# Optimization experiments

Hardware: AMD Instinct MI355X
Metric: run time of the kernel (lower is better)

Reference implementation:

```python
import jax, jax.numpy as jnp
import numpy as np

B, C, H, W = 8, 256, 64, 64
CR = C // 8  # reduced channels = 32


def setup_inputs() -> dict:
    key = jax.random.key(0)
    k1, k2, k3, k4 = jax.random.split(key, 4)
    x = jax.random.normal(k1, (B, C, H, W), dtype=jnp.float32)
    # 1x1 conv weights (bias=False) are plain channel matmuls; scale like kaiming (~1/sqrt(fan_in))
    Wt = jax.random.normal(k2, (3 * CR, C), dtype=jnp.float32) * (1.0 / np.sqrt(C))
    Wo = jax.random.normal(k3, (C, CR), dtype=jnp.float32) * (1.0 / np.sqrt(CR))
    scale = jax.random.normal(k4, (1,), dtype=jnp.float32)
    return {"x": x, "Wt": Wt, "Wo": Wo, "scale": scale}


def reference(x, Wt, Wo, scale):
    b, c, h, w = x.shape
    n = h * w
    # 1x1 conv QKV projection: [B, 3*Cr, H, W]
    t = jnp.einsum('oc,bchw->bohw', Wt, x)
    cr = t.shape[1] // 3
    key = t[:, :cr].reshape(b, cr, n)          # [B, Cr, N]
    query = t[:, cr:2 * cr].reshape(b, cr, n)  # [B, Cr, N]
    value = t[:, 2 * cr:].reshape(b, cr, n)    # [B, Cr, N]
    # scores[b, i, j] = sum_c key[b,c,i] * query[b,c,j]  (key^T @ query)
    scores = jnp.einsum('bci,bcj->bij', key, query)  # [B, N, N]
    # torch Softmax(dim=1): normalize over the key axis i
    weights = jax.nn.softmax(scores, axis=1)
    # output[b, c, j] = sum_i value[b,c,i] * weights[b,i,j]
    out = jnp.einsum('bci,bij->bcj', value, weights)  # [B, Cr, N]
    out = out.reshape(b, cr, h, w)
    out = jnp.einsum('oc,bchw->bohw', Wo, out)  # 1x1 conv back to C channels
    return scale[0] * out + x
```

## Files before the change

kernel.cpp:

```cpp
#include <hip/hip_runtime.h>
#include <math.h>

#define B_ 8
#define C_ 256
#define CR_ 32
#define N_ 4096
#define KSPLIT 8

typedef __attribute__((ext_vector_type(8))) short bf16x8;
typedef __attribute__((ext_vector_type(4))) short bf16x4;
typedef __attribute__((ext_vector_type(4))) float f32x4;
typedef __attribute__((ext_vector_type(16))) float f32x16;

__device__ inline short f2bf(float f) {
  union { float f; unsigned u; } v; v.f = f;
  unsigned r = v.u + 0x7FFFu + ((v.u >> 16) & 1u);
  return (short)(r >> 16);
}
__device__ inline float bf2f(short h) {
  union { unsigned u; float f; } v; v.u = ((unsigned)(unsigned short)h) << 16;
  return v.f;
}
__device__ inline short f2bf_r(float f) {
  return (short)((__float_as_uint(f) + 0x8000u) >> 16);
}

__global__ __launch_bounds__(256) void prep_weights(const float* __restrict__ Wt,
                                                    const float* __restrict__ Wo,
                                                    const float* __restrict__ scale,
                                                    short* __restrict__ WtHi,
                                                    short* __restrict__ WtLo,
                                                    short* __restrict__ WoB) {
  const int blk = blockIdx.x, tid = threadIdx.x;
  if (blk < 96) {
    float v = Wt[blk * C_ + tid];
    if (blk >= 32 && blk < 64) v *= 1.44269504f;
    const short h = f2bf(v);
    WtHi[blk * C_ + tid] = h;
    WtLo[blk * C_ + tid] = f2bf(v - bf2f(h));
  } else {
    const int idx = (blk - 96) * 256 + tid;
    WoB[idx] = f2bf(Wo[idx] * scale[0]);
  }
}

__global__ __launch_bounds__(256) void qkv_mfma(const float* __restrict__ x,
                                                const short* __restrict__ WtHi,
                                                const short* __restrict__ WtLo,
                                                short* __restrict__ t_tr,
                                                short* __restrict__ Vg) {
  const int b = blockIdx.y;
  const int tid = threadIdx.x;
  const int wave = tid >> 6, lane = tid & 63;
  const int pair = wave >> 1, chalf = wave & 1;
  const int col = lane & 15, quad = lane >> 4;
  const int n0 = (blockIdx.x * 2 + pair) * 16;
  const int cbase = chalf * 128;

  __shared__ float Ms[2][64][25];

  const f32x4 z4 = {0.f, 0.f, 0.f, 0.f};
  f32x4 acc[6] = {z4, z4, z4, z4, z4, z4};

  const float* xb = x + (size_t)b * C_ * N_ + n0 + col;
  float xcur[8], xnxt[8];
#pragma unroll
  for (int j = 0; j < 8; ++j) xcur[j] = xb[(size_t)(cbase + quad * 8 + j) * N_];

#pragma unroll
  for (int c0 = cbase; c0 < cbase + 128; c0 += 32) {
    if (c0 < cbase + 96) {
#pragma unroll
      for (int j = 0; j < 8; ++j)
        xnxt[j] = xb[(size_t)(c0 + 32 + quad * 8 + j) * N_];
    }
    bf16x8 xh, xl;
#pragma unroll
    for (int j = 0; j < 8; ++j) {
      const short h = (short)(__float_as_uint(xcur[j]) >> 16);
      xh[j] = h;
      xl[j] = f2bf_r(xcur[j] - bf2f(h));
    }
#pragma unroll
    for (int ot = 0; ot < 4; ++ot) {
      const int off = (ot * 16 + col) * C_ + c0 + quad * 8;
      const bf16x8 bh = *(const bf16x8*)(WtHi + off);
      const bf16x8 bl = *(const bf16x8*)(WtLo + off);
      acc[ot] = __builtin_amdgcn_mfma_f32_16x16x32_bf16(xh, bh, acc[ot], 0, 0, 0);
      acc[ot] = __builtin_amdgcn_mfma_f32_16x16x32_bf16(xl, bh, acc[ot], 0, 0, 0);
      acc[ot] = __builtin_amdgcn_mfma_f32_16x16x32_bf16(xh, bl, acc[ot], 0, 0, 0);
    }
#pragma unroll
    for (int ct = 0; ct < 2; ++ct) {
      const int off = ((64 + ct * 16) + col) * C_ + c0 + quad * 8;
      const bf16x8 ah = *(const bf16x8*)(WtHi + off);
      const bf16x8 al = *(const bf16x8*)(WtLo + off);
      acc[4 + ct] = __builtin_amdgcn_mfma_f32_16x16x32_bf16(ah, xh, acc[4 + ct], 0, 0, 0);
      acc[4 + ct] = __builtin_amdgcn_mfma_f32_16x16x32_bf16(ah, xl, acc[4 + ct], 0, 0, 0);
      acc[4 + ct] = __builtin_amdgcn_mfma_f32_16x16x32_bf16(al, xh, acc[4 + ct], 0, 0, 0);
    }
#pragma unroll
    for (int j = 0; j < 8; ++j) xcur[j] = xnxt[j];
  }

  if (chalf) {
    float* dst = &Ms[pair][lane][0];
#pragma unroll
    for (int t = 0; t < 6; ++t)
#pragma unroll
      for (int r = 0; r < 4; ++r) dst[t * 4 + r] = acc[t][r];
  }
  __syncthreads();
  if (!chalf) {
    const float* src = &Ms[pair][lane][0];
#pragma unroll
    for (int t = 0; t < 6; ++t)
#pragma unroll
      for (int r = 0; r < 4; ++r) acc[t][r] += src[t * 4 + r];
#pragma unroll
    for (int ot = 0; ot < 4; ++ot)
#pragma unroll
      for (int r = 0; r < 4; ++r)
        t_tr[((size_t)b * N_ + n0 + quad * 4 + r) * 64 + ot * 16 + col] =
            f2bf(acc[ot][r]);
#pragma unroll
    for (int ct = 0; ct < 2; ++ct)
#pragma unroll
      for (int r = 0; r < 4; ++r)
        Vg[(size_t)b * CR_ * N_ + (size_t)(ct * 16 + quad * 4 + r) * N_ + n0 + col] =
            f2bf(acc[4 + ct][r]);
  }
}

__global__ __launch_bounds__(64, 3) void flash_attn(const short* __restrict__ t_tr,
                                                    const short* __restrict__ Vg,
                                                    short* __restrict__ OPart,
                                                    float* __restrict__ LPart) {
  const int b = blockIdx.z, hq = blockIdx.y;
  const int j0 = blockIdx.x * 64;
  const int lane = threadIdx.x;
  const int j32 = lane & 31, h32 = lane >> 5;
  const short* T = t_tr + (size_t)b * N_ * 64;
  const short* V = Vg + (size_t)b * CR_ * N_;

  const f32x16 z16 = {0.f};
  bf16x8 qf[2][2];
#pragma unroll
  for (int jt = 0; jt < 2; ++jt)
#pragma unroll
    for (int ch = 0; ch < 2; ++ch)
      qf[jt][ch] = *(const bf16x8*)(T + (size_t)(j0 + jt * 32 + j32) * 64 + 32 +
                                    ch * 16 + h32 * 8);

  f32x16 acc[2] = {z16, z16};
  float ps[2] = {0.f, 0.f};

  const int ibase = hq * (N_ / KSPLIT);
  int i0 = ibase;
  bf16x8 kf[4], kfn[4];
#pragma unroll
  for (int it = 0; it < 2; ++it)
#pragma unroll
    for (int ch = 0; ch < 2; ++ch)
      kf[it * 2 + ch] = *(const bf16x8*)(T + (size_t)(ibase + it * 32 + j32) * 64 +
                                         ch * 16 + h32 * 8);

  for (int iter = 0; iter < 8; ++iter) {
    const int inx = ibase + ((iter + 1) & 7) * 64;
    bf16x8 vf[4];
#pragma unroll
    for (int ich = 0; ich < 4; ++ich)
      vf[ich] = *(const bf16x8*)(V + (size_t)j32 * N_ + i0 + ich * 16 + h32 * 8);
#pragma unroll
    for (int it = 0; it < 2; ++it)
#pragma unroll
      for (int ch = 0; ch < 2; ++ch)
        kfn[it * 2 + ch] = *(const bf16x8*)(T + (size_t)(inx + it * 32 + j32) * 64 +
                                            ch * 16 + h32 * 8);

#pragma unroll
    for (int it = 0; it < 2; ++it) {
#pragma unroll
      for (int jt = 0; jt < 2; ++jt) {
        f32x16 s = __builtin_amdgcn_mfma_f32_32x32x16_bf16(kf[it * 2 + 0], qf[jt][0], z16, 0, 0, 0);
        s = __builtin_amdgcn_mfma_f32_32x32x16_bf16(kf[it * 2 + 1], qf[jt][1], s, 0, 0, 0);
        float p[16];
#pragma unroll
        for (int r = 0; r < 16; ++r) p[r] = __builtin_amdgcn_exp2f(s[r]);
        ps[jt] += (((p[0] + p[1]) + (p[2] + p[3])) + ((p[4] + p[5]) + (p[6] + p[7]))) +
                  (((p[8] + p[9]) + (p[10] + p[11])) + ((p[12] + p[13]) + (p[14] + p[15])));
        unsigned d[8], xw[8];
#pragma unroll
        for (int k = 0; k < 8; ++k) {
          const unsigned u0 = __float_as_uint(p[2 * k]) + 0x8000u;
          const unsigned u1 = __float_as_uint(p[2 * k + 1]) + 0x8000u;
          d[k] = __builtin_amdgcn_perm(u1, u0, 0x07060302u);
        }
#pragma unroll
        for (int k = 0; k < 8; ++k) xw[k] = __shfl_xor((int)d[k], 32);
        union { unsigned u[4]; bf16x8 v; } f0, f1;
        f0.u[0] = h32 ? xw[2] : d[0];
        f0.u[1] = h32 ? xw[3] : d[1];
        f0.u[2] = h32 ? d[2] : xw[0];
        f0.u[3] = h32 ? d[3] : xw[1];
        f1.u[0] = h32 ? xw[6] : d[4];
        f1.u[1] = h32 ? xw[7] : d[5];
        f1.u[2] = h32 ? d[6] : xw[4];
        f1.u[3] = h32 ? d[7] : xw[5];
        acc[jt] = __builtin_amdgcn_mfma_f32_32x32x16_bf16(vf[it * 2 + 0], f0.v, acc[jt], 0, 0, 0);
        acc[jt] = __builtin_amdgcn_mfma_f32_32x32x16_bf16(vf[it * 2 + 1], f1.v, acc[jt], 0, 0, 0);
      }
    }
    i0 = inx;
#pragma unroll
    for (int k = 0; k < 4; ++k) kf[k] = kfn[k];
  }

  const size_t base = ((size_t)b * KSPLIT + hq) * N_;
#pragma unroll
  for (int jt = 0; jt < 2; ++jt) {
    const float l = ps[jt] + __shfl_xor(ps[jt], 32);
    const int jg = j0 + jt * 32 + j32;
    if (h32 == 0) LPart[base + jg] = l;
    short* OP = OPart + (base + jg) * 32;
#pragma unroll
    for (int g = 0; g < 4; ++g) {
      bf16x4 o = {f2bf(acc[jt][4 * g + 0]), f2bf(acc[jt][4 * g + 1]),
                  f2bf(acc[jt][4 * g + 2]), f2bf(acc[jt][4 * g + 3])};
      *(bf16x4*)(OP + 8 * g + 4 * h32) = o;
    }
  }
}

__global__ __launch_bounds__(256) void out_proj(const short* __restrict__ OPart,
                                                const float* __restrict__ LPart,
                                                const short* __restrict__ WoB,
                                                const float* __restrict__ x,
                                                float* __restrict__ out) {
  const int b = blockIdx.z, chalf = blockIdx.y;
  const int tid = threadIdx.x;
  const int wave = tid >> 6, lane = tid & 63;
  const int col = lane & 15, quad = lane >> 4;
  const int n0 = blockIdx.x * 64 + wave * 16;
  const int jg = n0 + col;
  const int coL = lane >> 2, n4 = lane & 3;

  __shared__ float Ls[4][2][16][20];

  float osum[8];
#pragma unroll
  for (int e = 0; e < 8; ++e) osum[e] = 0.f;
  float lsum = 0.f;
#pragma unroll
  for (int h = 0; h < KSPLIT; ++h) {
    const size_t p = ((size_t)b * KSPLIT + h) * N_ + jg;
    const bf16x8 o = *(const bf16x8*)(OPart + p * 32 + quad * 8);
#pragma unroll
    for (int e = 0; e < 8; ++e) osum[e] += bf2f(o[e]);
    lsum += LPart[p];
  }
  const float linv = 1.f / lsum;
  bf16x8 bf;
#pragma unroll
  for (int e = 0; e < 8; ++e) bf[e] = f2bf(osum[e] * linv);

  const float* xb = x + (size_t)b * C_ * N_;
  float* ob = out + (size_t)b * C_ * N_;
  float4 xv[8];
#pragma unroll
  for (int ct = 0; ct < 8; ++ct) {
    const int ctg = chalf * 8 + ct;
    xv[ct] = *(const float4*)(xb + (size_t)(ctg * 16 + coL) * N_ + n0 + n4 * 4);
  }

  const f32x4 z4 = {0.f, 0.f, 0.f, 0.f};
#pragma unroll
  for (int ct = 0; ct < 8; ++ct) {
    const int ctg = chalf * 8 + ct;
    const bf16x8 af = *(const bf16x8*)(WoB + (ctg * 16 + col) * 32 + quad * 8);
    const f32x4 a = __builtin_amdgcn_mfma_f32_16x16x32_bf16(af, bf, z4, 0, 0, 0);
    float* L = &Ls[wave][ct & 1][0][0];
#pragma unroll
    for (int r = 0; r < 4; ++r) L[(quad * 4 + r) * 20 + col] = a[r];
    const float4 lv = *(const float4*)&Ls[wave][ct & 1][coL][n4 * 4];
    float4 o;
    o.x = lv.x + xv[ct].x;
    o.y = lv.y + xv[ct].y;
    o.z = lv.z + xv[ct].z;
    o.w = lv.w + xv[ct].w;
    *(float4*)(ob + (size_t)(ctg * 16 + coL) * N_ + n0 + n4 * 4) = o;
  }
}

extern "C" void kernel_launch(void* const* d_in, const int* in_sizes, int n_in,
                              void* d_out, int out_size, void* d_ws,
                              size_t ws_size, hipStream_t stream) {
  const float* x = (const float*)d_in[0];
  const float* Wt = (const float*)d_in[1];
  const float* Wo = (const float*)d_in[2];
  const float* scale = (const float*)d_in[3];
  float* out = (float*)d_out;

  short* OPart = (short*)d_ws;
  float* LPart = (float*)(OPart + (size_t)B_ * KSPLIT * N_ * 32);
  short* t_tr = (short*)(LPart + (size_t)B_ * KSPLIT * N_);
  short* Vg = t_tr + (size_t)B_ * N_ * 64;
  short* WtHi = Vg + (size_t)B_ * CR_ * N_;
  short* WtLo = WtHi + 96 * C_;
  short* WoB = WtLo + 96 * C_;

  prep_weights<<<dim3(128), 256, 0, stream>>>(Wt, Wo, scale, WtHi, WtLo, WoB);
  qkv_mfma<<<dim3(128, B_), 256, 0, stream>>>(x, WtHi, WtLo, t_tr, Vg);
  flash_attn<<<dim3(64, KSPLIT, B_), 64, 0, stream>>>(t_tr, Vg, OPart, LPart);
  out_proj<<<dim3(64, 2, B_), 256, 0, stream>>>(OPart, LPart, WoB, x, out);
}
```

Baseline: 158.6 us.

## Merge key-split attention partials in shared memory within one block

```diff
diff --git a/kernel.cpp b/kernel.cpp
--- a/kernel.cpp
+++ b/kernel.cpp
@@ -5,7 +5,6 @@
 #define C_ 256
 #define CR_ 32
 #define N_ 4096
-#define KSPLIT 8
 
 typedef __attribute__((ext_vector_type(8))) short bf16x8;
 typedef __attribute__((ext_vector_type(4))) short bf16x4;
@@ -132,17 +131,20 @@
   }
 }
 
-__global__ __launch_bounds__(64, 3) void flash_attn(const short* __restrict__ t_tr,
-                                                    const short* __restrict__ Vg,
-                                                    short* __restrict__ OPart,
-                                                    float* __restrict__ LPart) {
-  const int b = blockIdx.z, hq = blockIdx.y;
+__global__ __launch_bounds__(256, 3) void flash_attn(const short* __restrict__ t_tr,
+                                                     const short* __restrict__ Vg,
+                                                     short* __restrict__ attT) {
+  const int b = blockIdx.y;
   const int j0 = blockIdx.x * 64;
-  const int lane = threadIdx.x;
+  const int tid = threadIdx.x;
+  const int wave = tid >> 6, lane = tid & 63;
   const int j32 = lane & 31, h32 = lane >> 5;
   const short* T = t_tr + (size_t)b * N_ * 64;
   const short* V = Vg + (size_t)b * CR_ * N_;
 
+  __shared__ float Om[4][64][36];
+  __shared__ float Lm[4][64];
+
   const f32x16 z16 = {0.f};
   bf16x8 qf[2][2];
 #pragma unroll
@@ -155,29 +157,23 @@
   f32x16 acc[2] = {z16, z16};
   float ps[2] = {0.f, 0.f};
 
-  const int ibase = hq * (N_ / KSPLIT);
-  int i0 = ibase;
-  bf16x8 kf[4], kfn[4];
-#pragma unroll
-  for (int it = 0; it < 2; ++it)
-#pragma unroll
-    for (int ch = 0; ch < 2; ++ch)
-      kf[it * 2 + ch] = *(const bf16x8*)(T + (size_t)(ibase + it * 32 + j32) * 64 +
-                                         ch * 16 + h32 * 8);
-
-  for (int iter = 0; iter < 8; ++iter) {
-    const int inx = ibase + ((iter + 1) & 7) * 64;
-    bf16x8 vf[4];
+  const int ibase = wave * 1024;
+
+  bf16x8 kfA[4], vfA[4], kfB[4], vfB[4];
+  auto loadK = [&](bf16x8* kf, int i) {
+#pragma unroll
+    for (int it = 0; it < 2; ++it)
+#pragma unroll
+      for (int ch = 0; ch < 2; ++ch)
+        kf[it * 2 + ch] = *(const bf16x8*)(T + (size_t)(i + it * 32 + j32) * 64 +
+                                           ch * 16 + h32 * 8);
+  };
+  auto loadV = [&](bf16x8* vf, int i) {
 #pragma unroll
     for (int ich = 0; ich < 4; ++ich)
-      vf[ich] = *(const bf16x8*)(V + (size_t)j32 * N_ + i0 + ich * 16 + h32 * 8);
-#pragma unroll
-    for (int it = 0; it < 2; ++it)
-#pragma unroll
-      for (int ch = 0; ch < 2; ++ch)
-        kfn[it * 2 + ch] = *(const bf16x8*)(T + (size_t)(inx + it * 32 + j32) * 64 +
-                                            ch * 16 + h32 * 8);
-
+      vf[ich] = *(const bf16x8*)(V + (size_t)j32 * N_ + i + ich * 16 + h32 * 8);
+  };
+  auto compute = [&](const bf16x8* kf, const bf16x8* vf) {
 #pragma unroll
     for (int it = 0; it < 2; ++it) {
 #pragma unroll
@@ -211,29 +207,49 @@
         acc[jt] = __builtin_amdgcn_mfma_f32_32x32x16_bf16(vf[it * 2 + 1], f1.v, acc[jt], 0, 0, 0);
       }
     }
-    i0 = inx;
-#pragma unroll
-    for (int k = 0; k < 4; ++k) kf[k] = kfn[k];
-  }
-
-  const size_t base = ((size_t)b * KSPLIT + hq) * N_;
+  };
+
+  loadK(kfA, ibase);
+  loadV(vfA, ibase);
+  for (int iter = 0; iter < 16; iter += 2) {
+    const int iB = ibase + ((iter + 1) & 15) * 64;
+    loadK(kfB, iB);
+    loadV(vfB, iB);
+    compute(kfA, vfA);
+    const int iA = ibase + ((iter + 2) & 15) * 64;
+    loadK(kfA, iA);
+    loadV(vfA, iA);
+    compute(kfB, vfB);
+  }
+
 #pragma unroll
   for (int jt = 0; jt < 2; ++jt) {
     const float l = ps[jt] + __shfl_xor(ps[jt], 32);
-    const int jg = j0 + jt * 32 + j32;
-    if (h32 == 0) LPart[base + jg] = l;
-    short* OP = OPart + (base + jg) * 32;
-#pragma unroll
-    for (int g = 0; g < 4; ++g) {
-      bf16x4 o = {f2bf(acc[jt][4 * g + 0]), f2bf(acc[jt][4 * g + 1]),
-                  f2bf(acc[jt][4 * g + 2]), f2bf(acc[jt][4 * g + 3])};
-      *(bf16x4*)(OP + 8 * g + 4 * h32) = o;
-    }
-  }
-}
-
-__global__ __launch_bounds__(256) void out_proj(const short* __restrict__ OPart,
-                                                const float* __restrict__ LPart,
+    if (h32 == 0) Lm[wave][jt * 32 + j32] = l;
+    float* Or = &Om[wave][jt * 32 + j32][0];
+#pragma unroll
+    for (int g = 0; g < 4; ++g)
+      *(float4*)(Or + 8 * g + 4 * h32) =
+          make_float4(acc[jt][4 * g + 0], acc[jt][4 * g + 1],
+                      acc[jt][4 * g + 2], acc[jt][4 * g + 3]);
+  }
+  __syncthreads();
+  {
+    const int j = tid >> 2, c0 = (tid & 3) * 8;
+    const float linv =
+        1.f / (Lm[0][j] + Lm[1][j] + Lm[2][j] + Lm[3][j]);
+    bf16x8 o;
+#pragma unroll
+    for (int e = 0; e < 8; ++e) {
+      const float s = Om[0][j][c0 + e] + Om[1][j][c0 + e] +
+                      Om[2][j][c0 + e] + Om[3][j][c0 + e];
+      o[e] = f2bf(s * linv);
+    }
+    *(bf16x8*)(attT + ((size_t)b * N_ + j0 + j) * 32 + c0) = o;
+  }
+}
+
+__global__ __launch_bounds__(256) void out_proj(const short* __restrict__ attT,
                                                 const short* __restrict__ WoB,
                                                 const float* __restrict__ x,
                                                 float* __restrict__ out) {
@@ -242,27 +258,12 @@
   const int wave = tid >> 6, lane = tid & 63;
   const int col = lane & 15, quad = lane >> 4;
   const int n0 = blockIdx.x * 64 + wave * 16;
-  const int jg = n0 + col;
   const int coL = lane >> 2, n4 = lane & 3;
 
   __shared__ float Ls[4][2][16][20];
 
-  float osum[8];
-#pragma unroll
-  for (int e = 0; e < 8; ++e) osum[e] = 0.f;
-  float lsum = 0.f;
-#pragma unroll
-  for (int h = 0; h < KSPLIT; ++h) {
-    const size_t p = ((size_t)b * KSPLIT + h) * N_ + jg;
-    const bf16x8 o = *(const bf16x8*)(OPart + p * 32 + quad * 8);
-#pragma unroll
-    for (int e = 0; e < 8; ++e) osum[e] += bf2f(o[e]);
-    lsum += LPart[p];
-  }
-  const float linv = 1.f / lsum;
-  bf16x8 bf;
-#pragma unroll
-  for (int e = 0; e < 8; ++e) bf[e] = f2bf(osum[e] * linv);
+  const bf16x8 bf =
+      *(const bf16x8*)(attT + ((size_t)b * N_ + n0 + col) * 32 + quad * 8);
 
   const float* xb = x + (size_t)b * C_ * N_;
   float* ob = out + (size_t)b * C_ * N_;
@@ -301,9 +302,8 @@
   const float* scale = (const float*)d_in[3];
   float* out = (float*)d_out;
 
-  short* OPart = (short*)d_ws;
-  float* LPart = (float*)(OPart + (size_t)B_ * KSPLIT * N_ * 32);
-  short* t_tr = (short*)(LPart + (size_t)B_ * KSPLIT * N_);
+  short* attT = (short*)d_ws;
+  short* t_tr = attT + (size_t)B_ * N_ * CR_;
   short* Vg = t_tr + (size_t)B_ * N_ * 64;
   short* WtHi = Vg + (size_t)B_ * CR_ * N_;
   short* WtLo = WtHi + 96 * C_;
@@ -311,6 +311,6 @@
 
   prep_weights<<<dim3(128), 256, 0, stream>>>(Wt, Wo, scale, WtHi, WtLo, WoB);
   qkv_mfma<<<dim3(128, B_), 256, 0, stream>>>(x, WtHi, WtLo, t_tr, Vg);
-  flash_attn<<<dim3(64, KSPLIT, B_), 64, 0, stream>>>(t_tr, Vg, OPart, LPart);
-  out_proj<<<dim3(64, 2, B_), 256, 0, stream>>>(OPart, LPart, WoB, x, out);
-}
+  flash_attn<<<dim3(64, B_), 256, 0, stream>>>(t_tr, Vg, attT);
+  out_proj<<<dim3(64, 2, B_), 256, 0, stream>>>(attT, WoB, x, out);
+}
```

New measurement: 264.2 us. 1.67x slower.
